# Optimization experiments

Measured on AMD Instinct MI355X. Metric: run time of the kernel, lower is better.

The kernel has to match this reference:

```python
import jax, jax.numpy as jnp
import numpy as np

B, T, J = 64, 1024, 22
PARENTS = [0, 0, 1, 2, 3, 0, 5, 6, 7, 0, 9, 10, 11, 12, 11, 14, 15, 16, 11, 18, 19, 20]
SPARSE_JOINTS = [0, 4, 8, 13, 17, 21]
EE = tuple(SPARSE_JOINTS[1:])                       # end effectors (sparse_joints[1:])
NO_SPARSE = tuple(j for j in range(J) if j not in SPARSE_JOINTS)
LAMBDA_EE, LAMBDA_EE_REG = 1.0, 0.1
IDENT_DQ = np.array([1, 0, 0, 0, 0, 0, 0, 0], dtype=np.float32)


def _qconj(q):
    return q * jnp.array([1.0, -1.0, -1.0, -1.0], q.dtype)


def _qmul(a, b):
    aw, ax, ay, az = a[..., 0], a[..., 1], a[..., 2], a[..., 3]
    bw, bx, by, bz = b[..., 0], b[..., 1], b[..., 2], b[..., 3]
    return jnp.stack([
        aw * bw - ax * bx - ay * by - az * bz,
        aw * bx + ax * bw + ay * bz - az * by,
        aw * by - ax * bz + ay * bw + az * bx,
        aw * bz + ax * by - ay * bx + az * bw], axis=-1)


def _qrot(q, v):
    # rotate vector v by unit quaternion q
    qv = q[..., 1:]
    t = 2.0 * jnp.cross(qv, v)
    return v + q[..., :1] * t + jnp.cross(qv, t)


def _qmat(q):
    w, x, y, z = q[..., 0], q[..., 1], q[..., 2], q[..., 3]
    m = jnp.stack([
        1 - 2 * (y * y + z * z), 2 * (x * y - w * z), 2 * (x * z + w * y),
        2 * (x * y + w * z), 1 - 2 * (x * x + z * z), 2 * (y * z - w * x),
        2 * (x * z - w * y), 2 * (y * z + w * x), 1 - 2 * (x * x + y * y)], axis=-1)
    return m.reshape(m.shape[:-1] + (3, 3))


def _denorm_to_dq(x, mean, std, set_root_identity):
    # x: (B, J*8, T) channel-major dual quats -> (B, T, J, 8)
    x = x * std[None, :, None] + mean[None, :, None]
    if set_root_identity:
        x = x.at[:, :8, :].set(jnp.asarray(IDENT_DQ, x.dtype)[None, :, None])
    b, c, t = x.shape
    return x.reshape(b, c // 8, 8, t).transpose(0, 3, 1, 2)


def _local_rot_from_dq(dq):
    # skeleton_from_dual_quat: real part = global rotation; make local via parent gather
    qr = dq[..., :4]
    qr = qr / jnp.linalg.norm(qr, axis=-1, keepdims=True)
    parent = jnp.asarray(PARENTS)
    local = _qmul(_qconj(qr[:, :, parent, :]), qr)   # (B,T,J,4)
    # forward_ik overwrites root local rotation with identity
    local = local.at[:, :, 0, :].set(jnp.array([1.0, 0.0, 0.0, 0.0], dq.dtype))
    return local


def _fk(local_rot, offsets):
    # fk_2: sequential parent-indexed propagation; root global pos is zeros
    rots = [local_rot[:, :, 0]]
    poss = [jnp.zeros(local_rot.shape[:2] + (3,), local_rot.dtype)]
    for j in range(1, J):
        p = PARENTS[j]
        rots.append(_qmul(rots[p], local_rot[:, :, j]))
        poss.append(_qrot(rots[p], offsets[j]) + poss[p])
    grot = jnp.stack(rots, axis=2)          # (B,T,J,4)
    pos = jnp.stack(poss, axis=2)           # (B,T,J,3)
    return pos, _qmat(grot)                  # positions, (B,T,J,3,3) rot matrices


def setup_inputs() -> dict:
    key = jax.random.key(0)
    ks = jax.random.split(key, 7)
    C = J * 8
    return {
        "input": jax.random.normal(ks[0], (B, C, T), jnp.float32),
        "input_ik": jax.random.normal(ks[1], (B, C - 8, T), jnp.float32),
        "input_decoder": jax.random.normal(ks[2], (B, C, T), jnp.float32),
        "target": jax.random.normal(ks[3], (B, C, T), jnp.float32),
        "mean_dqs": 0.1 * jax.random.normal(ks[4], (C,), jnp.float32),
        "std_dqs": 0.5 + 0.5 * jax.random.uniform(ks[5], (C,), jnp.float32),
        "offsets": jax.random.normal(ks[6], (J, 3), jnp.float32),
    }


def reference(input, input_ik, input_decoder, target, mean_dqs, std_dqs, offsets):
    # prepend identity-slot for the root (8 zero channels), then denormalize
    dq_ik = jnp.concatenate([jnp.zeros_like(input_ik[:, :8, :]), input_ik], axis=1)
    dq_ik = _denorm_to_dq(dq_ik, mean_dqs, std_dqs, True)
    dq_dec = _denorm_to_dq(input_decoder, mean_dqs, std_dqs, True)
    dq_tgt = _denorm_to_dq(target, mean_dqs, std_dqs, False)

    r_ik = _local_rot_from_dq(dq_ik)
    r_dec = _local_rot_from_dq(dq_dec)
    r_tgt = _local_rot_from_dq(dq_tgt)

    pos, rm = _fk(r_ik, offsets)
    tpos, trm = _fk(r_tgt, offsets)
    dpos, drm = _fk(r_dec, offsets)

    ee = jnp.asarray(EE)
    ns = jnp.asarray(NO_SPARSE)
    mse = lambda a, b: jnp.mean((a - b) ** 2)
    loss_ee = mse(pos[:, :, ee], tpos[:, :, ee]) + mse(rm[:, :, ee], trm[:, :, ee])
    loss_reg = mse(dpos[:, :, ns], pos[:, :, ns]) + mse(drm[:, :, ns], rm[:, :, ns])
    return loss_ee * LAMBDA_EE + loss_reg * LAMBDA_EE_REG
```

## Files before the change

### kernel.cpp

```cpp
#include <hip/hip_runtime.h>


#define T_DIM 1024

struct Q { float w, x, y, z; };
struct V3 { float x, y, z; };
struct St { Q rot; V3 pos; };

__device__ __forceinline__ Q qmul(const Q a, const Q b) {
    Q r;
    r.w = a.w*b.w - a.x*b.x - a.y*b.y - a.z*b.z;
    r.x = a.w*b.x + a.x*b.w + a.y*b.z - a.z*b.y;
    r.y = a.w*b.y - a.x*b.z + a.y*b.w + a.z*b.x;
    r.z = a.w*b.z + a.x*b.y - a.y*b.x + a.z*b.w;
    return r;
}

__device__ __forceinline__ V3 qrot(const Q q, const V3 v) {
    float tx = 2.f*(q.y*v.z - q.z*v.y);
    float ty = 2.f*(q.z*v.x - q.x*v.z);
    float tz = 2.f*(q.x*v.y - q.y*v.x);
    V3 r;
    r.x = v.x + q.w*tx + (q.y*tz - q.z*ty);
    r.y = v.y + q.w*ty + (q.z*tx - q.x*tz);
    r.z = v.z + q.w*tz + (q.x*ty - q.y*tx);
    return r;
}

__device__ __forceinline__ float rmdiff2u(const Q a, const Q b) {
    float d = a.w*b.w + a.x*b.x + a.y*b.y + a.z*b.z;
    return 8.f*(1.f - d*d);
}

__device__ __forceinline__ float pdiff2(const V3 a, const V3 b) {
    float dx=a.x-b.x, dy=a.y-b.y, dz=a.z-b.z;
    return dx*dx+dy*dy+dz*dz;
}

__device__ __forceinline__ V3 v3add(const V3 a, const V3 b) {
    return V3{a.x+b.x, a.y+b.y, a.z+b.z};
}

__device__ __forceinline__ Q mkq(const float r[4], const int c0,
                                 const float* __restrict__ mean,
                                 const float* __restrict__ stdv) {
    Q q;
    q.w = r[0]*stdv[c0+0] + mean[c0+0];
    q.x = r[1]*stdv[c0+1] + mean[c0+1];
    q.y = r[2]*stdv[c0+2] + mean[c0+2];
    q.z = r[3]*stdv[c0+3] + mean[c0+3];
    float inv = rsqrtf(q.w*q.w + q.x*q.x + q.y*q.y + q.z*q.z);
    q.w*=inv; q.x*=inv; q.y*=inv; q.z*=inv;
    return q;
}

template<int J0, int N>
__device__ __forceinline__ void pf2(
    const float* __restrict__ xp, const float* __restrict__ yp,
    float (*xr)[4], float (*yr)[4])
{
#pragma unroll
    for (int jj = 0; jj < N; ++jj) {
        const int j = J0 + jj;
#pragma unroll
        for (int c = 0; c < 4; ++c) {
            xr[jj][c] = xp[(j*8 + c)*T_DIM];
            yr[jj][c] = yp[(j*8 + c)*T_DIM];
        }
    }
}

template<int J, bool LOSS, bool PRE>
__device__ __forceinline__ void step2(
    St& sx, St& sy,
    const float xr[4], const float yr[4],
    const float* __restrict__ mean, const float* __restrict__ stdv,
    const float* __restrict__ offs, const Q q0c,
    float& ap, float& ar)
{
    const int c0 = J*8;
    Q qx = mkq(xr, c0, mean, stdv);
    Q qy = mkq(yr, c0, mean, stdv);
    if (PRE) qy = qmul(q0c, qy);
    V3 off = { offs[3*J], offs[3*J+1], offs[3*J+2] };
    V3 px = v3add(qrot(sx.rot, off), sx.pos);
    V3 py = v3add(qrot(sy.rot, off), sy.pos);
    if (LOSS) {
        ap += pdiff2(px, py);
        ar += rmdiff2u(qx, qy);
    }
    sx.rot = qx; sx.pos = px;
    sy.rot = qy; sy.pos = py;
}

template<bool EEROLE>
__device__ __forceinline__ void walk(
    const float* __restrict__ xp, const float* __restrict__ yp,
    const float* __restrict__ mean, const float* __restrict__ stdv,
    const float* __restrict__ offs,
    float& ap, float& ar)
{
    float Xa[4][4], Ya[4][4];
    float Xb[4][4], Yb[4][4];
    float Xc[5][4], Yc[5][4];
    float Xd[4][4], Yd[4][4];
    float Xe[4][4], Ye[4][4];
    float rq0[4];

    if (EEROLE) {
#pragma unroll
        for (int c = 0; c < 4; ++c) rq0[c] = yp[c*T_DIM];
    }
    pf2<1,4>(xp, yp, Xa, Ya);
    pf2<5,4>(xp, yp, Xb, Yb);

    Q q0c = {1.f, 0.f, 0.f, 0.f};
    if (EEROLE) {
        Q q0 = mkq(rq0, 0, mean, stdv);
        q0c = { q0.w, -q0.x, -q0.y, -q0.z };
    }
    const St root = { {1.f,0.f,0.f,0.f}, {0.f,0.f,0.f} };
    St sx, sy;

    sx = root; sy = root;
    step2<1, !EEROLE, EEROLE>(sx,sy, Xa[0],Ya[0], mean,stdv,offs,q0c, ap,ar);
    step2<2, !EEROLE, EEROLE>(sx,sy, Xa[1],Ya[1], mean,stdv,offs,q0c, ap,ar);
    step2<3, !EEROLE, EEROLE>(sx,sy, Xa[2],Ya[2], mean,stdv,offs,q0c, ap,ar);
    step2<4,  EEROLE, EEROLE>(sx,sy, Xa[3],Ya[3], mean,stdv,offs,q0c, ap,ar);

    pf2<9,5>(xp, yp, Xc, Yc);

    sx = root; sy = root;
    step2<5, !EEROLE, EEROLE>(sx,sy, Xb[0],Yb[0], mean,stdv,offs,q0c, ap,ar);
    step2<6, !EEROLE, EEROLE>(sx,sy, Xb[1],Yb[1], mean,stdv,offs,q0c, ap,ar);
    step2<7, !EEROLE, EEROLE>(sx,sy, Xb[2],Yb[2], mean,stdv,offs,q0c, ap,ar);
    step2<8,  EEROLE, EEROLE>(sx,sy, Xb[3],Yb[3], mean,stdv,offs,q0c, ap,ar);

    pf2<14,4>(xp, yp, Xd, Yd);

    sx = root; sy = root;
    step2<9,  !EEROLE, EEROLE>(sx,sy, Xc[0],Yc[0], mean,stdv,offs,q0c, ap,ar);
    step2<10, !EEROLE, EEROLE>(sx,sy, Xc[1],Yc[1], mean,stdv,offs,q0c, ap,ar);
    step2<11, !EEROLE, EEROLE>(sx,sy, Xc[2],Yc[2], mean,stdv,offs,q0c, ap,ar);
    const St sx11 = sx, sy11 = sy;
    step2<12, !EEROLE, EEROLE>(sx,sy, Xc[3],Yc[3], mean,stdv,offs,q0c, ap,ar);
    step2<13,  EEROLE, EEROLE>(sx,sy, Xc[4],Yc[4], mean,stdv,offs,q0c, ap,ar);

    pf2<18,4>(xp, yp, Xe, Ye);

    sx = sx11; sy = sy11;
    step2<14, !EEROLE, EEROLE>(sx,sy, Xd[0],Yd[0], mean,stdv,offs,q0c, ap,ar);
    step2<15, !EEROLE, EEROLE>(sx,sy, Xd[1],Yd[1], mean,stdv,offs,q0c, ap,ar);
    step2<16, !EEROLE, EEROLE>(sx,sy, Xd[2],Yd[2], mean,stdv,offs,q0c, ap,ar);
    step2<17,  EEROLE, EEROLE>(sx,sy, Xd[3],Yd[3], mean,stdv,offs,q0c, ap,ar);

    sx = sx11; sy = sy11;
    step2<18, !EEROLE, EEROLE>(sx,sy, Xe[0],Ye[0], mean,stdv,offs,q0c, ap,ar);
    step2<19, !EEROLE, EEROLE>(sx,sy, Xe[1],Ye[1], mean,stdv,offs,q0c, ap,ar);
    step2<20, !EEROLE, EEROLE>(sx,sy, Xe[2],Ye[2], mean,stdv,offs,q0c, ap,ar);
    step2<21,  EEROLE, EEROLE>(sx,sy, Xe[3],Ye[3], mean,stdv,offs,q0c, ap,ar);
}

__global__ __launch_bounds__(512, 1) void fk_loss_kernel(
    const float* __restrict__ ik, const float* __restrict__ dec,
    const float* __restrict__ tgt, const float* __restrict__ mean,
    const float* __restrict__ stdv, const float* __restrict__ offs,
    float* __restrict__ out)
{
    __shared__ float swred[8];
    const int tid = threadIdx.x;
    const int role = tid >> 8;
    const int lt = tid & 255;
    const int p = blockIdx.x * 256 + lt;
    const int b = p >> 10;
    const int t = p & 1023;
    const float* ikp = ik  + (size_t)b * (168*1024) + t - (size_t)(8*T_DIM);
    const float* dep = dec + (size_t)b * (176*1024) + t;
    const float* tgp = tgt + (size_t)b * (176*1024) + t;

    float ap = 0.f, ar = 0.f;
    float loss;
    const float BT = 65536.f;
    if (role == 0) {
        walk<true>(ikp, tgp, mean, stdv, offs, ap, ar);
        loss = ap * (1.0f/(BT*15.f)) + ar * (1.0f/(BT*45.f));
    } else {
        walk<false>(dep, ikp, mean, stdv, offs, ap, ar);
        loss = ap * (0.1f/(BT*48.f)) + ar * (0.1f/(BT*144.f));
    }

#pragma unroll
    for (int o = 32; o > 0; o >>= 1) loss += __shfl_down(loss, o);
    if ((tid & 63) == 0) swred[tid >> 6] = loss;
    __syncthreads();
    if (tid == 0) {
        float s = 0.f;
#pragma unroll
        for (int i = 0; i < 8; ++i) s += swred[i];
        atomicAdd(out, s);
    }
}

extern "C" void kernel_launch(void* const* d_in, const int* in_sizes, int n_in,
                              void* d_out, int out_size, void* d_ws, size_t ws_size,
                              hipStream_t stream) {
    const float* ikx  = (const float*)d_in[1];
    const float* dec  = (const float*)d_in[2];
    const float* tgt  = (const float*)d_in[3];
    const float* mean = (const float*)d_in[4];
    const float* stdv = (const float*)d_in[5];
    const float* offs = (const float*)d_in[6];
    float* out = (float*)d_out;

    hipMemsetAsync(out, 0, sizeof(float), stream);
    fk_loss_kernel<<<256, 512, 0, stream>>>(ikx, dec, tgt, mean, stdv, offs, out);
}
```

Before: 197.5 us.

## Split FK walk into per-chain blocks with XCD-aware block mapping

Each block now processes a single kinematic chain for one role instead of one thread walking all five chains, which raises the grid from 256 to 2560 blocks of 256 threads. The goal is more parallelism and occupancy on a GPU that otherwise runs one 512-thread block per CU with long serial dependency chains. Chains 14-17 and 18-21 each recompute the shared prefix 9-11, which adds redundant loads and math. Block indices are remapped so that all chains of a pose block land on the same XCD, to improve L2 locality for the shared input rows.

```diff
diff --git a/kernel.cpp b/kernel.cpp
--- a/kernel.cpp
+++ b/kernel.cpp
@@ -54,38 +54,33 @@
     return q;
 }
 
-template<int J0, int N>
-__device__ __forceinline__ void pf2(
+__device__ __forceinline__ void pfj(
     const float* __restrict__ xp, const float* __restrict__ yp,
-    float (*xr)[4], float (*yr)[4])
-{
-#pragma unroll
-    for (int jj = 0; jj < N; ++jj) {
-        const int j = J0 + jj;
-#pragma unroll
-        for (int c = 0; c < 4; ++c) {
-            xr[jj][c] = xp[(j*8 + c)*T_DIM];
-            yr[jj][c] = yp[(j*8 + c)*T_DIM];
-        }
-    }
-}
-
-template<int J, bool LOSS, bool PRE>
+    const int j, float xr[4], float yr[4])
+{
+#pragma unroll
+    for (int c = 0; c < 4; ++c) {
+        xr[c] = xp[(j*8 + c)*T_DIM];
+        yr[c] = yp[(j*8 + c)*T_DIM];
+    }
+}
+
 __device__ __forceinline__ void step2(
     St& sx, St& sy,
-    const float xr[4], const float yr[4],
+    const float xr[4], const float yr[4], const int j,
+    const bool loss, const bool pre,
     const float* __restrict__ mean, const float* __restrict__ stdv,
     const float* __restrict__ offs, const Q q0c,
     float& ap, float& ar)
 {
-    const int c0 = J*8;
+    const int c0 = j*8;
     Q qx = mkq(xr, c0, mean, stdv);
     Q qy = mkq(yr, c0, mean, stdv);
-    if (PRE) qy = qmul(q0c, qy);
-    V3 off = { offs[3*J], offs[3*J+1], offs[3*J+2] };
+    if (pre) qy = qmul(q0c, qy);
+    V3 off = { offs[3*j], offs[3*j+1], offs[3*j+2] };
     V3 px = v3add(qrot(sx.rot, off), sx.pos);
     V3 py = v3add(qrot(sy.rot, off), sy.pos);
-    if (LOSS) {
+    if (loss) {
         ap += pdiff2(px, py);
         ar += rmdiff2u(qx, qy);
     }
@@ -93,85 +88,74 @@
     sy.rot = qy; sy.pos = py;
 }
 
-template<bool EEROLE>
-__device__ __forceinline__ void walk(
+template<bool EEROLE, int CH>
+__device__ __forceinline__ void chainwalk(
     const float* __restrict__ xp, const float* __restrict__ yp,
     const float* __restrict__ mean, const float* __restrict__ stdv,
     const float* __restrict__ offs,
     float& ap, float& ar)
 {
-    float Xa[4][4], Ya[4][4];
-    float Xb[4][4], Yb[4][4];
-    float Xc[5][4], Yc[5][4];
-    float Xd[4][4], Yd[4][4];
-    float Xe[4][4], Ye[4][4];
+    constexpr int  J0  = (CH==0)?1 : (CH==1)?5 : (CH==2)?9 : (CH==3)?14 : 18;
+    constexpr int  N   = (CH==2)?5 : 4;
+    constexpr bool PFX = (CH>=3);
+
     float rq0[4];
+    float Xp[3][4], Yp[3][4];
+    float X[5][4],  Y[5][4];
 
     if (EEROLE) {
 #pragma unroll
         for (int c = 0; c < 4; ++c) rq0[c] = yp[c*T_DIM];
     }
-    pf2<1,4>(xp, yp, Xa, Ya);
-    pf2<5,4>(xp, yp, Xb, Yb);
+    if (PFX) {
+#pragma unroll
+        for (int i = 0; i < 3; ++i) pfj(xp, yp, 9+i, Xp[i], Yp[i]);
+    }
+#pragma unroll
+    for (int i = 0; i < N; ++i) pfj(xp, yp, J0+i, X[i], Y[i]);
 
     Q q0c = {1.f, 0.f, 0.f, 0.f};
     if (EEROLE) {
         Q q0 = mkq(rq0, 0, mean, stdv);
         q0c = { q0.w, -q0.x, -q0.y, -q0.z };
     }
-    const St root = { {1.f,0.f,0.f,0.f}, {0.f,0.f,0.f} };
-    St sx, sy;
-
-    sx = root; sy = root;
-    step2<1, !EEROLE, EEROLE>(sx,sy, Xa[0],Ya[0], mean,stdv,offs,q0c, ap,ar);
-    step2<2, !EEROLE, EEROLE>(sx,sy, Xa[1],Ya[1], mean,stdv,offs,q0c, ap,ar);
-    step2<3, !EEROLE, EEROLE>(sx,sy, Xa[2],Ya[2], mean,stdv,offs,q0c, ap,ar);
-    step2<4,  EEROLE, EEROLE>(sx,sy, Xa[3],Ya[3], mean,stdv,offs,q0c, ap,ar);
-
-    pf2<9,5>(xp, yp, Xc, Yc);
-
-    sx = root; sy = root;
-    step2<5, !EEROLE, EEROLE>(sx,sy, Xb[0],Yb[0], mean,stdv,offs,q0c, ap,ar);
-    step2<6, !EEROLE, EEROLE>(sx,sy, Xb[1],Yb[1], mean,stdv,offs,q0c, ap,ar);
-    step2<7, !EEROLE, EEROLE>(sx,sy, Xb[2],Yb[2], mean,stdv,offs,q0c, ap,ar);
-    step2<8,  EEROLE, EEROLE>(sx,sy, Xb[3],Yb[3], mean,stdv,offs,q0c, ap,ar);
-
-    pf2<14,4>(xp, yp, Xd, Yd);
-
-    sx = root; sy = root;
-    step2<9,  !EEROLE, EEROLE>(sx,sy, Xc[0],Yc[0], mean,stdv,offs,q0c, ap,ar);
-    step2<10, !EEROLE, EEROLE>(sx,sy, Xc[1],Yc[1], mean,stdv,offs,q0c, ap,ar);
-    step2<11, !EEROLE, EEROLE>(sx,sy, Xc[2],Yc[2], mean,stdv,offs,q0c, ap,ar);
-    const St sx11 = sx, sy11 = sy;
-    step2<12, !EEROLE, EEROLE>(sx,sy, Xc[3],Yc[3], mean,stdv,offs,q0c, ap,ar);
-    step2<13,  EEROLE, EEROLE>(sx,sy, Xc[4],Yc[4], mean,stdv,offs,q0c, ap,ar);
-
-    pf2<18,4>(xp, yp, Xe, Ye);
-
-    sx = sx11; sy = sy11;
-    step2<14, !EEROLE, EEROLE>(sx,sy, Xd[0],Yd[0], mean,stdv,offs,q0c, ap,ar);
-    step2<15, !EEROLE, EEROLE>(sx,sy, Xd[1],Yd[1], mean,stdv,offs,q0c, ap,ar);
-    step2<16, !EEROLE, EEROLE>(sx,sy, Xd[2],Yd[2], mean,stdv,offs,q0c, ap,ar);
-    step2<17,  EEROLE, EEROLE>(sx,sy, Xd[3],Yd[3], mean,stdv,offs,q0c, ap,ar);
-
-    sx = sx11; sy = sy11;
-    step2<18, !EEROLE, EEROLE>(sx,sy, Xe[0],Ye[0], mean,stdv,offs,q0c, ap,ar);
-    step2<19, !EEROLE, EEROLE>(sx,sy, Xe[1],Ye[1], mean,stdv,offs,q0c, ap,ar);
-    step2<20, !EEROLE, EEROLE>(sx,sy, Xe[2],Ye[2], mean,stdv,offs,q0c, ap,ar);
-    step2<21,  EEROLE, EEROLE>(sx,sy, Xe[3],Ye[3], mean,stdv,offs,q0c, ap,ar);
-}
-
-__global__ __launch_bounds__(512, 1) void fk_loss_kernel(
+
+    St sx = { {1.f,0.f,0.f,0.f}, {0.f,0.f,0.f} };
+    St sy = sx;
+
+    if (PFX) {
+#pragma unroll
+        for (int i = 0; i < 3; ++i)
+            step2(sx, sy, Xp[i], Yp[i], 9+i, false, EEROLE,
+                  mean, stdv, offs, q0c, ap, ar);
+    }
+#pragma unroll
+    for (int i = 0; i < N; ++i) {
+        const bool loss = EEROLE ? (i == N-1) : (i != N-1);
+        step2(sx, sy, X[i], Y[i], J0+i, loss, EEROLE,
+              mean, stdv, offs, q0c, ap, ar);
+    }
+}
+
+__global__ __launch_bounds__(256) void fk_loss_kernel(
     const float* __restrict__ ik, const float* __restrict__ dec,
     const float* __restrict__ tgt, const float* __restrict__ mean,
     const float* __restrict__ stdv, const float* __restrict__ offs,
     float* __restrict__ out)
 {
-    __shared__ float swred[8];
+    __shared__ float swred[4];
     const int tid = threadIdx.x;
-    const int role = tid >> 8;
-    const int lt = tid & 255;
-    const int p = blockIdx.x * 256 + lt;
+
+    const int bid  = blockIdx.x;
+    const int xcd  = bid & 7;
+    const int idx  = bid >> 3;
+    const int pb   = idx / 10;
+    const int sub  = idx - pb*10;
+    const int pose_blk = xcd*32 + pb;
+    const int role  = (sub >= 5) ? 1 : 0;
+    const int chain = sub - role*5;
+
+    const int p = pose_blk*256 + tid;
     const int b = p >> 10;
     const int t = p & 1023;
     const float* ikp = ik  + (size_t)b * (168*1024) + t - (size_t)(8*T_DIM);
@@ -182,10 +166,22 @@
     float loss;
     const float BT = 65536.f;
     if (role == 0) {
-        walk<true>(ikp, tgp, mean, stdv, offs, ap, ar);
+        switch (chain) {
+            case 0: chainwalk<true,0>(ikp, tgp, mean, stdv, offs, ap, ar); break;
+            case 1: chainwalk<true,1>(ikp, tgp, mean, stdv, offs, ap, ar); break;
+            case 2: chainwalk<true,2>(ikp, tgp, mean, stdv, offs, ap, ar); break;
+            case 3: chainwalk<true,3>(ikp, tgp, mean, stdv, offs, ap, ar); break;
+            default: chainwalk<true,4>(ikp, tgp, mean, stdv, offs, ap, ar); break;
+        }
         loss = ap * (1.0f/(BT*15.f)) + ar * (1.0f/(BT*45.f));
     } else {
-        walk<false>(dep, ikp, mean, stdv, offs, ap, ar);
+        switch (chain) {
+            case 0: chainwalk<false,0>(dep, ikp, mean, stdv, offs, ap, ar); break;
+            case 1: chainwalk<false,1>(dep, ikp, mean, stdv, offs, ap, ar); break;
+            case 2: chainwalk<false,2>(dep, ikp, mean, stdv, offs, ap, ar); break;
+            case 3: chainwalk<false,3>(dep, ikp, mean, stdv, offs, ap, ar); break;
+            default: chainwalk<false,4>(dep, ikp, mean, stdv, offs, ap, ar); break;
+        }
         loss = ap * (0.1f/(BT*48.f)) + ar * (0.1f/(BT*144.f));
     }
 
@@ -194,10 +190,7 @@
     if ((tid & 63) == 0) swred[tid >> 6] = loss;
     __syncthreads();
     if (tid == 0) {
-        float s = 0.f;
-#pragma unroll
-        for (int i = 0; i < 8; ++i) s += swred[i];
-        atomicAdd(out, s);
+        atomicAdd(out, swred[0]+swred[1]+swred[2]+swred[3]);
     }
 }
 
@@ -213,5 +206,5 @@
     float* out = (float*)d_out;
 
     hipMemsetAsync(out, 0, sizeof(float), stream);
-    fk_loss_kernel<<<256, 512, 0, stream>>>(ikx, dec, tgt, mean, stdv, offs, out);
-}
+    fk_loss_kernel<<<2560, 256, 0, stream>>>(ikx, dec, tgt, mean, stdv, offs, out);
+}
```

Result: faster. 180.0 us (-8.9%).
